# Optimization experiments

Hardware: AMD Instinct MI355X
Metric: run time of the kernel (lower is better)

## Reference

```python
import jax, jax.numpy as jnp
import numpy as np

B_SZ, L_SEQ, D_MODEL, D_STATE = 4, 2048, 1024, 16


def setup_inputs() -> dict:
    key = jax.random.key(0)
    ks = jax.random.split(key, 6)
    x = jax.random.normal(ks[0], (B_SZ, L_SEQ, D_MODEL), jnp.float32)
    # HiPPO-inspired init: A_log = log(arange(1..n)).clamp(min=-7), broadcast over channels
    A_log = jnp.clip(jnp.log(jnp.arange(1, D_STATE + 1, dtype=jnp.float32)), -7.0, None)
    A_log = jnp.broadcast_to(A_log[None, :], (D_MODEL, D_STATE)).astype(jnp.float32)
    B_param = 0.02 * jax.random.normal(ks[1], (D_MODEL, D_STATE), jnp.float32)
    C_param = 0.02 * jax.random.normal(ks[2], (D_MODEL, D_STATE), jnp.float32)
    log_dt = 0.01 * jax.random.normal(ks[3], (D_MODEL,), jnp.float32) - 4.0
    in_w = jax.random.normal(ks[4], (2 * D_MODEL, D_MODEL), jnp.float32) / np.sqrt(D_MODEL).astype(np.float32)
    in_b = jnp.zeros((2 * D_MODEL,), jnp.float32)
    out_w = jax.random.normal(ks[5], (D_MODEL, D_MODEL), jnp.float32) / np.sqrt(D_MODEL).astype(np.float32)
    out_b = jnp.zeros((D_MODEL,), jnp.float32)
    ln_g = jnp.ones((D_MODEL,), jnp.float32)
    ln_b = jnp.zeros((D_MODEL,), jnp.float32)
    return {"x": x, "A_log": A_log, "B_param": B_param, "C_param": C_param,
            "log_dt": log_dt, "in_w": in_w, "in_b": in_b, "out_w": out_w,
            "out_b": out_b, "ln_g": ln_g, "ln_b": ln_b}


def _ssm_scan(u, A_log, B_param, C_param, log_dt):
    # u: (B, L, D). Builds kernel h[t,d] = sum_n A_bar[d,n]^t * C[d,n]*B[d,n]*dt[d]
    # and applies a causal depthwise convolution (via FFT; same math as conv1d).
    L = u.shape[1]
    dt = jnp.clip(jnp.exp(log_dt), 1e-4, 1.0)                      # (D,)
    A_bar = jnp.exp(-jnp.exp(A_log) * dt[:, None])                 # ZOH discretisation (D,N)
    A_bar = jnp.clip(A_bar, 1e-8, 1.0 - 1e-8)
    log_A = jnp.log(A_bar)                                         # (D,N)
    t_idx = jnp.arange(L, dtype=jnp.float32)                       # (L,)
    A_powers = jnp.exp(t_idx[:, None, None] * log_A[None, :, :])   # (L,D,N)
    cb_dt = C_param * B_param * dt[:, None]                        # (D,N)
    kernel = jnp.einsum('ldn,dn->ld', A_powers, cb_dt)             # (L,D)
    # causal conv: y[b,t,d] = sum_{tau<=t} kernel[tau,d] * u[b,t-tau,d]
    n_fft = 2 * L
    Kf = jnp.fft.rfft(kernel, n=n_fft, axis=0)                     # (n_fft/2+1, D)
    Uf = jnp.fft.rfft(u, n=n_fft, axis=1)                          # (B, n_fft/2+1, D)
    y = jnp.fft.irfft(Uf * Kf[None], n=n_fft, axis=1)[:, :L]       # (B,L,D)
    return y.astype(u.dtype)


def reference(x, A_log, B_param, C_param, log_dt, in_w, in_b, out_w, out_b, ln_g, ln_b):
    x = x.astype(jnp.float32)
    residual = x
    # LayerNorm (eps=1e-5)
    mu = jnp.mean(x, axis=-1, keepdims=True)
    var = jnp.mean(jnp.square(x - mu), axis=-1, keepdims=True)
    xn = (x - mu) * jax.lax.rsqrt(var + 1e-5) * ln_g + ln_b
    xz = xn @ in_w.T + in_b                                        # (B,L,2D)
    x_proj, z = xz[..., :D_MODEL], xz[..., D_MODEL:]
    z = jax.nn.silu(z)
    y = _ssm_scan(x_proj, A_log, B_param, C_param, log_dt)
    y = y * z
    y = y @ out_w.T + out_b
    # dropout is identity in eval mode
    return jnp.clip(y + residual, -10.0, 10.0)
```

## Files before the change

### kernel.cpp

```cpp
#include <hip/hip_runtime.h>
#include <hip/hip_bf16.h>

#define D_MODEL 1024
#define D_STATE 16
#define L_SEQ 2048
#define B_SZ 4
#define M_ROWS (B_SZ * L_SEQ)
#define N_CHUNK 32
#define C_LEN 64

typedef __attribute__((ext_vector_type(8))) short short8;
typedef __attribute__((ext_vector_type(4))) float f32x4;
typedef unsigned int u32;
#define GLOBAL_AS __attribute__((address_space(1)))
#define LDS_AS __attribute__((address_space(3)))

static __device__ __forceinline__ unsigned short f2bf(float f) {
    unsigned int u = __float_as_uint(f);
    unsigned int r = (u + 0x7FFFu + ((u >> 16) & 1u)) >> 16;
    return (unsigned short)r;
}
static __device__ __forceinline__ float bf2f(unsigned short u) {
    return __uint_as_float(((unsigned int)u) << 16);
}

__global__ void conv_bf16_kernel(const float* __restrict__ src,
                                 unsigned short* __restrict__ dst, int n4) {
    int i = blockIdx.x * blockDim.x + threadIdx.x;
    if (i < n4) {
        float4 v = ((const float4*)src)[i];
        ushort4 o;
        o.x = f2bf(v.x); o.y = f2bf(v.y); o.z = f2bf(v.z); o.w = f2bf(v.w);
        ((ushort4*)dst)[i] = o;
    }
}

__global__ __launch_bounds__(256) void ln_kernel(const float* __restrict__ x,
                                                 const float* __restrict__ g,
                                                 const float* __restrict__ b,
                                                 unsigned short* __restrict__ xn) {
    int row = blockIdx.x;
    int t = threadIdx.x;
    const float4* xr = (const float4*)(x + (size_t)row * D_MODEL);
    float4 v = xr[t];
    float s  = v.x + v.y + v.z + v.w;
    float ss = v.x * v.x + v.y * v.y + v.z * v.z + v.w * v.w;
    #pragma unroll
    for (int o = 32; o > 0; o >>= 1) {
        s  += __shfl_down(s,  o);
        ss += __shfl_down(ss, o);
    }
    __shared__ float sbuf[8];
    int wid = t >> 6;
    if ((t & 63) == 0) { sbuf[wid] = s; sbuf[4 + wid] = ss; }
    __syncthreads();
    float S  = sbuf[0] + sbuf[1] + sbuf[2] + sbuf[3];
    float SS = sbuf[4] + sbuf[5] + sbuf[6] + sbuf[7];
    float mu  = S * (1.0f / D_MODEL);
    float var = SS * (1.0f / D_MODEL) - mu * mu;
    float inv = rsqrtf(var + 1e-5f);
    float4 gv = ((const float4*)g)[t];
    float4 bv = ((const float4*)b)[t];
    ushort4 o;
    o.x = f2bf((v.x - mu) * inv * gv.x + bv.x);
    o.y = f2bf((v.y - mu) * inv * gv.y + bv.y);
    o.z = f2bf((v.z - mu) * inv * gv.z + bv.z);
    o.w = f2bf((v.w - mu) * inv * gv.w + bv.w);
    ((ushort4*)(xn + (size_t)row * D_MODEL))[t] = o;
}

template<int MODE>
__global__ __launch_bounds__(256) void gemm_kernel(const unsigned short* __restrict__ A,
                                                   const unsigned short* __restrict__ Bt,
                                                   const float* __restrict__ bias,
                                                   float* __restrict__ out_f,
                                                   unsigned short* __restrict__ out_bf,
                                                   const float* __restrict__ resid,
                                                   int K) {
    __shared__ unsigned short lA[128 * 32];
    __shared__ unsigned short lB[128 * 32];

    int t = threadIdx.x;
    int lane = t & 63;
    int wave = t >> 6;
    int wm = wave >> 1, wn = wave & 1;
    int m0 = blockIdx.y * 128;
    int n0 = blockIdx.x * 128;
    int row = lane & 15;
    int quad = lane >> 4;

    int sr = t >> 2;
    int sc = ((t & 3) ^ ((t >> 3) & 3)) * 8;
    const unsigned short* gA0 = A + (size_t)(m0 + sr) * K + sc;
    const unsigned short* gA1 = A + (size_t)(m0 + 64 + sr) * K + sc;
    const unsigned short* gB0 = Bt + (size_t)(n0 + sr) * K + sc;
    const unsigned short* gB1 = Bt + (size_t)(n0 + 64 + sr) * K + sc;

    int offA[4], offB[4];
    #pragma unroll
    for (int i = 0; i < 4; i++) {
        int r6 = i * 16 + row;
        int slotA = r6 * 4 + (quad ^ ((r6 >> 1) & 3));
        offA[i] = wm * 2048 + slotA * 8;
        offB[i] = wn * 2048 + slotA * 8;
    }

    f32x4 acc[4][4] = {};

    for (int kk = 0; kk < K; kk += 32) {
        __builtin_amdgcn_global_load_lds((const GLOBAL_AS u32*)(gA0 + kk),
                                         (LDS_AS u32*)&lA[t * 8], 16, 0, 0);
        __builtin_amdgcn_global_load_lds((const GLOBAL_AS u32*)(gA1 + kk),
                                         (LDS_AS u32*)&lA[2048 + t * 8], 16, 0, 0);
        __builtin_amdgcn_global_load_lds((const GLOBAL_AS u32*)(gB0 + kk),
                                         (LDS_AS u32*)&lB[t * 8], 16, 0, 0);
        __builtin_amdgcn_global_load_lds((const GLOBAL_AS u32*)(gB1 + kk),
                                         (LDS_AS u32*)&lB[2048 + t * 8], 16, 0, 0);
        __syncthreads();

        short8 a[4], b[4];
        #pragma unroll
        for (int i = 0; i < 4; i++) a[i] = *(const short8*)&lA[offA[i]];
        #pragma unroll
        for (int j = 0; j < 4; j++) b[j] = *(const short8*)&lB[offB[j]];
        #pragma unroll
        for (int i = 0; i < 4; i++)
            #pragma unroll
            for (int j = 0; j < 4; j++)
                acc[i][j] = __builtin_amdgcn_mfma_f32_16x16x32_bf16(a[i], b[j], acc[i][j], 0, 0, 0);
        __syncthreads();
    }

    int col = row;
    #pragma unroll
    for (int i = 0; i < 4; i++) {
        #pragma unroll
        for (int j = 0; j < 4; j++) {
            int n = n0 + wn * 64 + j * 16 + col;
            float bs = bias[n];
            #pragma unroll
            for (int r = 0; r < 4; r++) {
                int m = m0 + wm * 64 + i * 16 + quad * 4 + r;
                float v = acc[i][j][r] + bs;
                if (MODE == 1) {
                    if (n < D_MODEL) {
                        out_f[(size_t)m * D_MODEL + n] = v;
                    } else {
                        float sv = v / (1.0f + __expf(-v));
                        out_bf[(size_t)m * D_MODEL + (n - D_MODEL)] = f2bf(sv);
                    }
                } else {
                    float y = v + resid[(size_t)m * D_MODEL + n];
                    y = fminf(10.0f, fmaxf(-10.0f, y));
                    out_f[(size_t)m * D_MODEL + n] = y;
                }
            }
        }
    }
}

static __device__ __forceinline__ void load_params(const float* __restrict__ A_log,
                                                   const float* __restrict__ log_dt,
                                                   int d, float* ab, float& dt_out) {
    float dt = fminf(1.0f, fmaxf(1e-4f, __expf(log_dt[d])));
    #pragma unroll
    for (int n = 0; n < D_STATE; n++) {
        float a = __expf(-__expf(A_log[d * D_STATE + n]) * dt);
        ab[n] = fminf(1.0f - 1e-8f, fmaxf(1e-8f, a));
    }
    dt_out = dt;
}

__global__ __launch_bounds__(256) void scan1_kernel(const float* __restrict__ u,
                                                    const float* __restrict__ A_log,
                                                    const float* __restrict__ log_dt,
                                                    float* __restrict__ s_local) {
    int gid = blockIdx.x * 256 + threadIdx.x;
    int d = gid & (D_MODEL - 1);
    int c = (gid >> 10) & (N_CHUNK - 1);
    int b = gid >> 15;

    float ab[D_STATE], dt;
    load_params(A_log, log_dt, d, ab, dt);

    float s[D_STATE];
    #pragma unroll
    for (int n = 0; n < D_STATE; n++) s[n] = 0.0f;

    const float* up = u + ((size_t)(b * L_SEQ + c * C_LEN)) * D_MODEL + d;
    for (int t = 0; t < C_LEN; t++) {
        float uv = up[(size_t)t * D_MODEL];
        #pragma unroll
        for (int n = 0; n < D_STATE; n++) s[n] = fmaf(ab[n], s[n], uv);
    }
    float* sl = s_local + ((size_t)(b * N_CHUNK + c) * D_STATE) * D_MODEL + d;
    #pragma unroll
    for (int n = 0; n < D_STATE; n++) sl[(size_t)n * D_MODEL] = s[n];
}

__global__ __launch_bounds__(256) void scan_combine_kernel(const float* __restrict__ s_local,
                                                           const float* __restrict__ A_log,
                                                           const float* __restrict__ log_dt,
                                                           float* __restrict__ s_init) {
    int gid = blockIdx.x * 256 + threadIdx.x;
    int d = gid & (D_MODEL - 1);
    int n = (gid >> 10) & (D_STATE - 1);
    int b = gid >> 14;

    float dt = fminf(1.0f, fmaxf(1e-4f, __expf(log_dt[d])));
    float a = __expf(-__expf(A_log[d * D_STATE + n]) * dt);
    a = fminf(1.0f - 1e-8f, fmaxf(1e-8f, a));
    float aP = a;
    #pragma unroll
    for (int q = 0; q < 6; q++) aP = aP * aP;

    float s = 0.0f;
    size_t stride_c = (size_t)D_STATE * D_MODEL;
    const float* sl = s_local + ((size_t)b * N_CHUNK * D_STATE + n) * D_MODEL + d;
    float* si = s_init + ((size_t)b * N_CHUNK * D_STATE + n) * D_MODEL + d;
    si[0] = 0.0f;
    for (int c = 1; c < N_CHUNK; c++) {
        s = fmaf(aP, s, sl[(size_t)(c - 1) * stride_c]);
        si[(size_t)c * stride_c] = s;
    }
}

__global__ __launch_bounds__(256) void scan2_kernel(const float* __restrict__ u,
                                                    const unsigned short* __restrict__ zs,
                                                    const float* __restrict__ A_log,
                                                    const float* __restrict__ Bp,
                                                    const float* __restrict__ Cp,
                                                    const float* __restrict__ log_dt,
                                                    const float* __restrict__ s_init,
                                                    unsigned short* __restrict__ yz) {
    int gid = blockIdx.x * 256 + threadIdx.x;
    int d = gid & (D_MODEL - 1);
    int c = (gid >> 10) & (N_CHUNK - 1);
    int b = gid >> 15;

    float ab[D_STATE], dt;
    load_params(A_log, log_dt, d, ab, dt);
    float cb[D_STATE];
    #pragma unroll
    for (int n = 0; n < D_STATE; n++)
        cb[n] = Cp[d * D_STATE + n] * Bp[d * D_STATE + n] * dt;

    float s[D_STATE];
    const float* si = s_init + ((size_t)(b * N_CHUNK + c) * D_STATE) * D_MODEL + d;
    #pragma unroll
    for (int n = 0; n < D_STATE; n++) s[n] = si[(size_t)n * D_MODEL];

    size_t m0 = (size_t)(b * L_SEQ + c * C_LEN);
    const float* up = u + m0 * D_MODEL + d;
    const unsigned short* zp = zs + m0 * D_MODEL + d;
    unsigned short* yp = yz + m0 * D_MODEL + d;

    for (int t = 0; t < C_LEN; t++) {
        float uv = up[(size_t)t * D_MODEL];
        #pragma unroll
        for (int n = 0; n < D_STATE; n++) s[n] = fmaf(ab[n], s[n], uv);
        float y = 0.0f;
        #pragma unroll
        for (int n = 0; n < D_STATE; n++) y = fmaf(cb[n], s[n], y);
        float zv = bf2f(zp[(size_t)t * D_MODEL]);
        yp[(size_t)t * D_MODEL] = f2bf(y * zv);
    }
}

extern "C" void kernel_launch(void* const* d_in, const int* in_sizes, int n_in,
                              void* d_out, int out_size, void* d_ws, size_t ws_size,
                              hipStream_t stream) {
    const float* x       = (const float*)d_in[0];
    const float* A_log   = (const float*)d_in[1];
    const float* B_param = (const float*)d_in[2];
    const float* C_param = (const float*)d_in[3];
    const float* log_dt  = (const float*)d_in[4];
    const float* in_w    = (const float*)d_in[5];
    const float* in_b    = (const float*)d_in[6];
    const float* out_w   = (const float*)d_in[7];
    const float* out_b   = (const float*)d_in[8];
    const float* ln_g    = (const float*)d_in[9];
    const float* ln_b    = (const float*)d_in[10];
    float* out = (float*)d_out;

    char* ws = (char*)d_ws;
    size_t off = 0;
    unsigned short* xn = (unsigned short*)(ws + off); off += (size_t)M_ROWS * D_MODEL * 2;
    unsigned short* w1 = (unsigned short*)(ws + off); off += (size_t)2 * D_MODEL * D_MODEL * 2;
    float*          u  = (float*)(ws + off);          off += (size_t)M_ROWS * D_MODEL * 4;
    unsigned short* zs = (unsigned short*)(ws + off); off += (size_t)M_ROWS * D_MODEL * 2;
    unsigned short* yz = (unsigned short*)(ws + off); off += (size_t)M_ROWS * D_MODEL * 2;
    unsigned short* w2 = (unsigned short*)(ws + off); off += (size_t)D_MODEL * D_MODEL * 2;
    float* s_local = (float*)(ws + off); off += (size_t)B_SZ * N_CHUNK * D_STATE * D_MODEL * 4;
    float* s_init  = (float*)(ws + off); off += (size_t)B_SZ * N_CHUNK * D_STATE * D_MODEL * 4;

    {
        int n4 = 2 * D_MODEL * D_MODEL / 4;
        conv_bf16_kernel<<<(n4 + 255) / 256, 256, 0, stream>>>(in_w, w1, n4);
    }
    {
        int n4 = D_MODEL * D_MODEL / 4;
        conv_bf16_kernel<<<(n4 + 255) / 256, 256, 0, stream>>>(out_w, w2, n4);
    }

    ln_kernel<<<M_ROWS, 256, 0, stream>>>(x, ln_g, ln_b, xn);

    gemm_kernel<1><<<dim3(2 * D_MODEL / 128, M_ROWS / 128), 256, 0, stream>>>(
        xn, w1, in_b, u, zs, nullptr, D_MODEL);

    scan1_kernel<<<(B_SZ * N_CHUNK * D_MODEL) / 256, 256, 0, stream>>>(u, A_log, log_dt, s_local);
    scan_combine_kernel<<<(B_SZ * D_STATE * D_MODEL) / 256, 256, 0, stream>>>(s_local, A_log, log_dt, s_init);
    scan2_kernel<<<(B_SZ * N_CHUNK * D_MODEL) / 256, 256, 0, stream>>>(
        u, zs, A_log, B_param, C_param, log_dt, s_init, yz);

    gemm_kernel<2><<<dim3(D_MODEL / 128, M_ROWS / 128), 256, 0, stream>>>(
        yz, w2, out_b, out, nullptr, x, D_MODEL);
}
```

Baseline: 240.5 us.

## Widen in-projection GEMM tile to 128x256 and store u in bf16

Splits the templated GEMM into two kernels. The in-projection GEMM now uses a 128x256 output tile with a 4x8 MFMA accumulator per wave, which raises reuse of each A fragment and halves the number of blocks. The intermediate u is now written as bf16 instead of fp32, which halves the write traffic from the GEMM and the read traffic in both scan kernels. The larger tile raises register and LDS pressure, and bf16 u reduces the precision of the scan input.

```diff
diff --git a/kernel.cpp b/kernel.cpp
--- a/kernel.cpp
+++ b/kernel.cpp
@@ -69,16 +69,108 @@
     ((ushort4*)(xn + (size_t)row * D_MODEL))[t] = o;
 }
 
-template<int MODE>
-__global__ __launch_bounds__(256) void gemm_kernel(const unsigned short* __restrict__ A,
-                                                   const unsigned short* __restrict__ Bt,
-                                                   const float* __restrict__ bias,
-                                                   float* __restrict__ out_f,
-                                                   unsigned short* __restrict__ out_bf,
-                                                   const float* __restrict__ resid,
-                                                   int K) {
+__global__ __launch_bounds__(256, 2) void gemm1_kernel(const unsigned short* __restrict__ A,
+                                                       const unsigned short* __restrict__ Bt,
+                                                       const float* __restrict__ bias,
+                                                       unsigned short* __restrict__ u_bf,
+                                                       unsigned short* __restrict__ zs) {
+    __shared__ unsigned short lA[128 * 32];
+    __shared__ unsigned short lB[256 * 32];
+    const int K = D_MODEL;
+
+    int t = threadIdx.x;
+    int lane = t & 63;
+    int wave = t >> 6;
+    int wm = wave >> 1, wn = wave & 1;
+    int m0 = blockIdx.y * 128;
+    int n0 = blockIdx.x * 256;
+    int row = lane & 15;
+    int quad = lane >> 4;
+
+    int sr = t >> 2;
+    int sc = ((t & 3) ^ ((t >> 3) & 3)) * 8;
+    const unsigned short* gA0 = A + (size_t)(m0 + sr) * K + sc;
+    const unsigned short* gA1 = A + (size_t)(m0 + 64 + sr) * K + sc;
+    const unsigned short* gB0 = Bt + (size_t)(n0 + sr) * K + sc;
+    const unsigned short* gB1 = Bt + (size_t)(n0 + 64 + sr) * K + sc;
+    const unsigned short* gB2 = Bt + (size_t)(n0 + 128 + sr) * K + sc;
+    const unsigned short* gB3 = Bt + (size_t)(n0 + 192 + sr) * K + sc;
+
+    int offA[4], offB[8];
+    #pragma unroll
+    for (int i = 0; i < 4; i++) {
+        int r6 = i * 16 + row;
+        int slot = r6 * 4 + (quad ^ ((r6 >> 1) & 3));
+        offA[i] = wm * 2048 + slot * 8;
+    }
+    #pragma unroll
+    for (int j = 0; j < 8; j++) {
+        int r8 = wn * 128 + j * 16 + row;
+        int half = r8 >> 6, r6 = r8 & 63;
+        int slot = r6 * 4 + (quad ^ ((r6 >> 1) & 3));
+        offB[j] = half * 2048 + slot * 8;
+    }
+
+    f32x4 acc[4][8] = {};
+
+    for (int kk = 0; kk < K; kk += 32) {
+        __builtin_amdgcn_global_load_lds((const GLOBAL_AS u32*)(gA0 + kk),
+                                         (LDS_AS u32*)&lA[t * 8], 16, 0, 0);
+        __builtin_amdgcn_global_load_lds((const GLOBAL_AS u32*)(gA1 + kk),
+                                         (LDS_AS u32*)&lA[2048 + t * 8], 16, 0, 0);
+        __builtin_amdgcn_global_load_lds((const GLOBAL_AS u32*)(gB0 + kk),
+                                         (LDS_AS u32*)&lB[t * 8], 16, 0, 0);
+        __builtin_amdgcn_global_load_lds((const GLOBAL_AS u32*)(gB1 + kk),
+                                         (LDS_AS u32*)&lB[2048 + t * 8], 16, 0, 0);
+        __builtin_amdgcn_global_load_lds((const GLOBAL_AS u32*)(gB2 + kk),
+                                         (LDS_AS u32*)&lB[4096 + t * 8], 16, 0, 0);
+        __builtin_amdgcn_global_load_lds((const GLOBAL_AS u32*)(gB3 + kk),
+                                         (LDS_AS u32*)&lB[6144 + t * 8], 16, 0, 0);
+        __syncthreads();
+
+        short8 a[4];
+        #pragma unroll
+        for (int i = 0; i < 4; i++) a[i] = *(const short8*)&lA[offA[i]];
+        #pragma unroll
+        for (int j = 0; j < 8; j++) {
+            short8 b = *(const short8*)&lB[offB[j]];
+            #pragma unroll
+            for (int i = 0; i < 4; i++)
+                acc[i][j] = __builtin_amdgcn_mfma_f32_16x16x32_bf16(a[i], b, acc[i][j], 0, 0, 0);
+        }
+        __syncthreads();
+    }
+
+    int col = row;
+    #pragma unroll
+    for (int j = 0; j < 8; j++) {
+        int n = n0 + wn * 128 + j * 16 + col;
+        float bs = bias[n];
+        #pragma unroll
+        for (int i = 0; i < 4; i++) {
+            #pragma unroll
+            for (int r = 0; r < 4; r++) {
+                int m = m0 + wm * 64 + i * 16 + quad * 4 + r;
+                float v = acc[i][j][r] + bs;
+                if (n < D_MODEL) {
+                    u_bf[(size_t)m * D_MODEL + n] = f2bf(v);
+                } else {
+                    float sv = v / (1.0f + __expf(-v));
+                    zs[(size_t)m * D_MODEL + (n - D_MODEL)] = f2bf(sv);
+                }
+            }
+        }
+    }
+}
+
+__global__ __launch_bounds__(256) void gemm2_kernel(const unsigned short* __restrict__ A,
+                                                    const unsigned short* __restrict__ Bt,
+                                                    const float* __restrict__ bias,
+                                                    float* __restrict__ out_f,
+                                                    const float* __restrict__ resid) {
     __shared__ unsigned short lA[128 * 32];
     __shared__ unsigned short lB[128 * 32];
+    const int K = D_MODEL;
 
     int t = threadIdx.x;
     int lane = t & 63;
@@ -100,9 +192,9 @@
     #pragma unroll
     for (int i = 0; i < 4; i++) {
         int r6 = i * 16 + row;
-        int slotA = r6 * 4 + (quad ^ ((r6 >> 1) & 3));
-        offA[i] = wm * 2048 + slotA * 8;
-        offB[i] = wn * 2048 + slotA * 8;
+        int slot = r6 * 4 + (quad ^ ((r6 >> 1) & 3));
+        offA[i] = wm * 2048 + slot * 8;
+        offB[i] = wn * 2048 + slot * 8;
     }
 
     f32x4 acc[4][4] = {};
@@ -141,19 +233,9 @@
             #pragma unroll
             for (int r = 0; r < 4; r++) {
                 int m = m0 + wm * 64 + i * 16 + quad * 4 + r;
-                float v = acc[i][j][r] + bs;
-                if (MODE == 1) {
-                    if (n < D_MODEL) {
-                        out_f[(size_t)m * D_MODEL + n] = v;
-                    } else {
-                        float sv = v / (1.0f + __expf(-v));
-                        out_bf[(size_t)m * D_MODEL + (n - D_MODEL)] = f2bf(sv);
-                    }
-                } else {
-                    float y = v + resid[(size_t)m * D_MODEL + n];
-                    y = fminf(10.0f, fmaxf(-10.0f, y));
-                    out_f[(size_t)m * D_MODEL + n] = y;
-                }
+                float y = acc[i][j][r] + bs + resid[(size_t)m * D_MODEL + n];
+                y = fminf(10.0f, fmaxf(-10.0f, y));
+                out_f[(size_t)m * D_MODEL + n] = y;
             }
         }
     }
@@ -171,7 +253,7 @@
     dt_out = dt;
 }
 
-__global__ __launch_bounds__(256) void scan1_kernel(const float* __restrict__ u,
+__global__ __launch_bounds__(256) void scan1_kernel(const unsigned short* __restrict__ u,
                                                     const float* __restrict__ A_log,
                                                     const float* __restrict__ log_dt,
                                                     float* __restrict__ s_local) {
@@ -187,9 +269,9 @@
     #pragma unroll
     for (int n = 0; n < D_STATE; n++) s[n] = 0.0f;
 
-    const float* up = u + ((size_t)(b * L_SEQ + c * C_LEN)) * D_MODEL + d;
+    const unsigned short* up = u + ((size_t)(b * L_SEQ + c * C_LEN)) * D_MODEL + d;
     for (int t = 0; t < C_LEN; t++) {
-        float uv = up[(size_t)t * D_MODEL];
+        float uv = bf2f(up[(size_t)t * D_MODEL]);
         #pragma unroll
         for (int n = 0; n < D_STATE; n++) s[n] = fmaf(ab[n], s[n], uv);
     }
@@ -225,7 +307,7 @@
     }
 }
 
-__global__ __launch_bounds__(256) void scan2_kernel(const float* __restrict__ u,
+__global__ __launch_bounds__(256) void scan2_kernel(const unsigned short* __restrict__ u,
                                                     const unsigned short* __restrict__ zs,
                                                     const float* __restrict__ A_log,
                                                     const float* __restrict__ Bp,
@@ -251,12 +333,12 @@
     for (int n = 0; n < D_STATE; n++) s[n] = si[(size_t)n * D_MODEL];
 
     size_t m0 = (size_t)(b * L_SEQ + c * C_LEN);
-    const float* up = u + m0 * D_MODEL + d;
+    const unsigned short* up = u + m0 * D_MODEL + d;
     const unsigned short* zp = zs + m0 * D_MODEL + d;
     unsigned short* yp = yz + m0 * D_MODEL + d;
 
     for (int t = 0; t < C_LEN; t++) {
-        float uv = up[(size_t)t * D_MODEL];
+        float uv = bf2f(up[(size_t)t * D_MODEL]);
         #pragma unroll
         for (int n = 0; n < D_STATE; n++) s[n] = fmaf(ab[n], s[n], uv);
         float y = 0.0f;
@@ -287,7 +369,7 @@
     size_t off = 0;
     unsigned short* xn = (unsigned short*)(ws + off); off += (size_t)M_ROWS * D_MODEL * 2;
     unsigned short* w1 = (unsigned short*)(ws + off); off += (size_t)2 * D_MODEL * D_MODEL * 2;
-    float*          u  = (float*)(ws + off);          off += (size_t)M_ROWS * D_MODEL * 4;
+    unsigned short* u  = (unsigned short*)(ws + off); off += (size_t)M_ROWS * D_MODEL * 2;
     unsigned short* zs = (unsigned short*)(ws + off); off += (size_t)M_ROWS * D_MODEL * 2;
     unsigned short* yz = (unsigned short*)(ws + off); off += (size_t)M_ROWS * D_MODEL * 2;
     unsigned short* w2 = (unsigned short*)(ws + off); off += (size_t)D_MODEL * D_MODEL * 2;
@@ -305,14 +387,14 @@
 
     ln_kernel<<<M_ROWS, 256, 0, stream>>>(x, ln_g, ln_b, xn);
 
-    gemm_kernel<1><<<dim3(2 * D_MODEL / 128, M_ROWS / 128), 256, 0, stream>>>(
-        xn, w1, in_b, u, zs, nullptr, D_MODEL);
+    gemm1_kernel<<<dim3(2 * D_MODEL / 256, M_ROWS / 128), 256, 0, stream>>>(
+        xn, w1, in_b, u, zs);
 
     scan1_kernel<<<(B_SZ * N_CHUNK * D_MODEL) / 256, 256, 0, stream>>>(u, A_log, log_dt, s_local);
     scan_combine_kernel<<<(B_SZ * D_STATE * D_MODEL) / 256, 256, 0, stream>>>(s_local, A_log, log_dt, s_init);
     scan2_kernel<<<(B_SZ * N_CHUNK * D_MODEL) / 256, 256, 0, stream>>>(
         u, zs, A_log, B_param, C_param, log_dt, s_init, yz);
 
-    gemm_kernel<2><<<dim3(D_MODEL / 128, M_ROWS / 128), 256, 0, stream>>>(
-        yz, w2, out_b, out, nullptr, x, D_MODEL);
-}
+    gemm2_kernel<<<dim3(D_MODEL / 128, M_ROWS / 128), 256, 0, stream>>>(
+        yz, w2, out_b, out, x);
+}
```

Result: faster. 223.0 us (-7.3%).
